# Kernel tuning notes

Hardware: AMD Instinct MI355X
Metric: run time of the kernel (lower is better)

The kernel has to match this reference:

```python
import jax, jax.numpy as jnp
import numpy as np

N_NODES = 40000
N_EDGES = 640000
D = 128
NEG_SLOPE = 0.2
EPS = 0.0  # init_eps=0, learn_eps=False -> constant buffer


def setup_inputs() -> dict:
    key = jax.random.key(0)
    ks = jax.random.split(key, 9)
    return {
        "feat": jax.random.normal(ks[0], (N_NODES, D), dtype=jnp.float32),
        "W_src": jax.random.normal(ks[1], (D, D), dtype=jnp.float32) * 0.1,
        "W_dst": jax.random.normal(ks[2], (D, D), dtype=jnp.float32) * 0.1,
        "W_src2": jax.random.normal(ks[3], (D, D), dtype=jnp.float32) * 0.1,
        "W_dst2": jax.random.normal(ks[4], (D, D), dtype=jnp.float32) * 0.1,
        "attn_l": jax.random.normal(ks[5], (D,), dtype=jnp.float32) * 0.1,
        "attn_r": jax.random.normal(ks[6], (D,), dtype=jnp.float32) * 0.1,
        "src": jax.random.randint(ks[7], (N_EDGES,), 0, N_NODES, dtype=jnp.int32),
        "dst": jax.random.randint(ks[8], (N_EDGES,), 0, N_NODES, dtype=jnp.int32),
    }


def reference(feat, W_src, W_dst, W_src2, W_dst2, attn_l, attn_r, src, dst):
    n = feat.shape[0]
    # Four linear projections (no bias), nn.Linear applies x @ W.T
    fs1 = feat @ W_src.T    # [N, D] -> messages for GIN sum
    fd1 = feat @ W_dst.T    # [N, D] -> self term
    fs2 = feat @ W_src2.T   # [N, D] -> attention-weighted messages
    fd2 = feat @ W_dst2.T   # [N, D]

    # GAT-style per-node attention logits
    el = jnp.sum(fs2 * attn_l, axis=-1)  # [N]
    er = jnp.sum(fd2 * attn_r, axis=-1)  # [N]

    # Per-edge score: u_add_v + leaky_relu
    e = el[src] + er[dst]                                   # [E]
    e = jnp.where(e >= 0, e, NEG_SLOPE * e)

    # edge_softmax: segment-wise softmax over edges grouped by dst
    seg_max = jax.ops.segment_max(e, dst, num_segments=n)   # [N]
    seg_max = jnp.where(jnp.isfinite(seg_max), seg_max, 0.0)
    ex = jnp.exp(e - seg_max[dst])                          # [E]
    denom = jax.ops.segment_sum(ex, dst, num_segments=n)    # [N]
    a = ex / denom[dst]                                     # [E]

    # update_all(copy_u, sum): plain neighbor sum of fs1
    neigh = jax.ops.segment_sum(fs1[src], dst, num_segments=n)            # [N, D]
    # update_all(u_mul_e, sum): attention-weighted sum of fs2
    add_ft = jax.ops.segment_sum(fs2[src] * a[:, None], dst, num_segments=n)  # [N, D]

    rst = (1.0 + EPS) * fd1 + neigh + add_ft
    return rst
```

## Files before the change

kernel.cpp:

```cpp
#include <hip/hip_runtime.h>
#include <math.h>

#define N_NODES 40000
#define N_EDGES 640000
#define D 128
#define NEG_SLOPE 0.2f
#define BCAP 64

typedef __bf16 bf16x8 __attribute__((ext_vector_type(8)));
typedef float f32x4 __attribute__((ext_vector_type(4)));

__device__ __forceinline__ unsigned short f2bf(float f) {
    unsigned int u = __float_as_uint(f);
    return (unsigned short)((u + 0x7fffu + ((u >> 16) & 1u)) >> 16);
}

__global__ void k_init_fill(const float* __restrict__ Ws, const float* __restrict__ Ws2,
                            const float* __restrict__ Wd, const float* __restrict__ Wd2,
                            const float* __restrict__ attn_l, const float* __restrict__ attn_r,
                            unsigned short* __restrict__ Wfrag,
                            float* __restrict__ v_l, float* __restrict__ v_r,
                            const int* __restrict__ src, const int* __restrict__ dst,
                            int* __restrict__ cnt, unsigned short* __restrict__ bucket) {
    if (blockIdx.x >= 193) {
        int e = (blockIdx.x - 193) * 256 + threadIdx.x;
        if (e < N_EDGES) {
            int d = dst[e];
            int slot = atomicAdd(&cnt[d], 1);
            if (slot < BCAP) bucket[(size_t)d * BCAP + slot] = (unsigned short)src[e];
        }
        return;
    }
    if (blockIdx.x == 192) {
        int t = threadIdx.x;
        if (t < 128) {
            float s = 0.0f;
            for (int j = 0; j < D; ++j) s += attn_l[j] * Ws2[j * D + t];
            v_l[t] = s;
        } else {
            int k = t - 128;
            float s = 0.0f;
            for (int j = 0; j < D; ++j) s += attn_r[j] * Wd2[j * D + k];
            v_r[k] = s;
        }
        return;
    }
    int idx = blockIdx.x * 256 + threadIdx.x;
    int e    = idx & 7;
    int lane = (idx >> 3) & 63;
    int ks   = (idx >> 9) & 3;
    int ct   = (idx >> 11) & 7;
    int m    = idx >> 14;
    int col  = ct * 16 + (lane & 15);
    int k    = ks * 32 + (lane >> 4) * 8 + e;
    const float* W = (m == 0) ? Ws : (m == 1) ? Ws2 : Wd;
    Wfrag[idx] = f2bf(W[col * D + k]);
}

__global__ __launch_bounds__(256) void k_gemm(
    const float* __restrict__ feat, const unsigned short* __restrict__ Wfrag,
    const float* __restrict__ vl, const float* __restrict__ vr,
    unsigned int* __restrict__ fsc, unsigned short* __restrict__ fd1b,
    float* __restrict__ el, float* __restrict__ er)
{
    const int m    = blockIdx.x / 625;
    const int tile = blockIdx.x % 625;
    const int lane = threadIdx.x & 63;
    const int wave = threadIdx.x >> 6;
    const int row0 = tile * 64 + wave * 16;
    const int arow = row0 + (lane & 15);
    const int kb   = (lane >> 4) * 8;

    bf16x8 a[4];
    float sl = 0.f, sr = 0.f;
    #pragma unroll
    for (int ks = 0; ks < 4; ++ks) {
        const float* fp = feat + (size_t)arow * D + ks * 32 + kb;
        float4 p = *(const float4*)fp;
        float4 q = *(const float4*)(fp + 4);
        bf16x8 av;
        av[0] = (__bf16)p.x; av[1] = (__bf16)p.y; av[2] = (__bf16)p.z; av[3] = (__bf16)p.w;
        av[4] = (__bf16)q.x; av[5] = (__bf16)q.y; av[6] = (__bf16)q.z; av[7] = (__bf16)q.w;
        a[ks] = av;
        if (m == 0) {
            const float* vlp = vl + ks * 32 + kb;
            const float* vrp = vr + ks * 32 + kb;
            float4 l0 = *(const float4*)vlp, l1 = *(const float4*)(vlp + 4);
            float4 r0 = *(const float4*)vrp, r1 = *(const float4*)(vrp + 4);
            sl += p.x*l0.x + p.y*l0.y + p.z*l0.z + p.w*l0.w
                + q.x*l1.x + q.y*l1.y + q.z*l1.z + q.w*l1.w;
            sr += p.x*r0.x + p.y*r0.y + p.z*r0.z + p.w*r0.w
                + q.x*r1.x + q.y*r1.y + q.z*r1.z + q.w*r1.w;
        }
    }
    if (m == 0) {
        sl += __shfl_xor(sl, 16); sl += __shfl_xor(sl, 32);
        sr += __shfl_xor(sr, 16); sr += __shfl_xor(sr, 32);
        if (lane < 16) { el[row0 + lane] = sl; er[row0 + lane] = sr; }
    }

    const bf16x8* wf = (const bf16x8*)Wfrag + (size_t)(m * 8 * 4) * 64;
    f32x4 acc[8];
    #pragma unroll
    for (int ct = 0; ct < 8; ++ct) acc[ct] = (f32x4){0.f, 0.f, 0.f, 0.f};
    #pragma unroll
    for (int ks = 0; ks < 4; ++ks) {
        #pragma unroll
        for (int ct = 0; ct < 8; ++ct) {
            bf16x8 b = wf[(size_t)(ct * 4 + ks) * 64 + lane];
            acc[ct] = __builtin_amdgcn_mfma_f32_16x16x32_bf16(a[ks], b, acc[ct], 0, 0, 0);
        }
    }

    const int rbase = row0 + (lane >> 4) * 4;
    const int cbase = lane & 15;
    if (m == 2) {
        #pragma unroll
        for (int ct = 0; ct < 8; ++ct)
            #pragma unroll
            for (int r = 0; r < 4; ++r)
                fd1b[(size_t)(rbase + r) * D + ct * 16 + cbase] = f2bf(acc[ct][r]);
    } else {
        const int codd = cbase & 1;
        #pragma unroll
        for (int ct = 0; ct < 8; ++ct) {
            #pragma unroll
            for (int r = 0; r < 4; ++r) {
                unsigned int x = (unsigned int)f2bf(acc[ct][r]);
                unsigned int y = __shfl_xor(x, 1);
                if (!codd) {
                    unsigned int wrd = (y << 16) | x;
                    fsc[(size_t)(rbase + r) * 128 + ct * 16 + cbase + m] = wrd;
                }
            }
        }
    }
}

__global__ __launch_bounds__(256) void k_aggregate(
    const int* __restrict__ cnt, const unsigned short* __restrict__ bucket,
    const float* __restrict__ el, const float* __restrict__ er,
    const uint2* __restrict__ fsc, const unsigned short* __restrict__ fd1b,
    float* __restrict__ out)
{
    const int node = blockIdx.x * 4 + (threadIdx.x >> 6);
    const int lane = threadIdx.x & 63;
    if (node >= N_NODES) return;
    int deg = cnt[node];
    deg = (deg > BCAP) ? BCAP : deg;

    unsigned int u0 = *(const unsigned int*)(fd1b + (size_t)node * D + lane * 2);
    float accx = __uint_as_float(u0 << 16);
    float accy = __uint_as_float(u0 & 0xffff0000u);

    if (deg > 0) {
        const int base = node * BCAP;
        const float ern = er[node];
        int s_l = 0;
        float e = -INFINITY;
        if (lane < deg) {
            s_l = bucket[base + lane];
            e = el[s_l] + ern;
            e = (e >= 0.f) ? e : NEG_SLOPE * e;
        }
        float mx = e;
        #pragma unroll
        for (int w = 32; w >= 1; w >>= 1) mx = fmaxf(mx, __shfl_xor(mx, w));
        float p = (lane < deg) ? __expf(e - mx) : 0.f;
        float ssum = p;
        #pragma unroll
        for (int w = 32; w >= 1; w >>= 1) ssum += __shfl_xor(ssum, w);
        float a_l = p / ssum;

        const int dup = (deg + 15) & ~15;
        for (int i = 0; i < dup; i += 16) {
            uint2 q[16];
            float av[16];
            #pragma unroll
            for (int j = 0; j < 16; ++j) {
                int s = __shfl(s_l, i + j);
                av[j] = __shfl(a_l, i + j);
                q[j] = fsc[(size_t)s * 64 + lane];
            }
            #pragma unroll
            for (int j = 0; j < 16; ++j) {
                float wf = (i + j < deg) ? 1.0f : 0.0f;
                accx += wf * __uint_as_float(q[j].x << 16) + av[j] * __uint_as_float(q[j].y << 16);
                accy += wf * __uint_as_float(q[j].x & 0xffff0000u) + av[j] * __uint_as_float(q[j].y & 0xffff0000u);
            }
        }
    }

    *(float2*)(out + (size_t)node * D + lane * 2) = make_float2(accx, accy);
}

extern "C" void kernel_launch(void* const* d_in, const int* in_sizes, int n_in,
                              void* d_out, int out_size, void* d_ws, size_t ws_size,
                              hipStream_t stream) {
    const float* feat   = (const float*)d_in[0];
    const float* W_src  = (const float*)d_in[1];
    const float* W_dst  = (const float*)d_in[2];
    const float* W_src2 = (const float*)d_in[3];
    const float* W_dst2 = (const float*)d_in[4];
    const float* attn_l = (const float*)d_in[5];
    const float* attn_r = (const float*)d_in[6];
    const int*   src    = (const int*)d_in[7];
    const int*   dst    = (const int*)d_in[8];
    float* out = (float*)d_out;

    char* w = (char*)d_ws;
    float* v_l = (float*)w;                       w += 128 * 4;
    float* v_r = (float*)w;                       w += 128 * 4;
    float* el  = (float*)w;                       w += N_NODES * 4;
    float* er  = (float*)w;                       w += N_NODES * 4;
    int* cnt   = (int*)w;                         w += N_NODES * 4;
    unsigned int* fsc = (unsigned int*)w;         w += (size_t)N_NODES * 128 * 4;
    unsigned short* fd1b = (unsigned short*)w;    w += (size_t)N_NODES * D * 2;
    unsigned short* bucket = (unsigned short*)w;  w += (size_t)N_NODES * BCAP * 2;
    unsigned short* Wfrag = (unsigned short*)w;   w += 3 * 8 * 4 * 64 * 8 * 2;

    hipMemsetAsync(cnt, 0, N_NODES * sizeof(int), stream);

    k_init_fill<<<193 + (N_EDGES + 255) / 256, 256, 0, stream>>>(
        W_src, W_src2, W_dst, W_dst2, attn_l, attn_r, Wfrag, v_l, v_r,
        src, dst, cnt, bucket);

    k_gemm<<<1875, 256, 0, stream>>>(feat, Wfrag, v_l, v_r, fsc, fd1b, el, er);

    k_aggregate<<<(N_NODES + 3) / 4, 256, 0, stream>>>(cnt, bucket, el, er,
                                                       (const uint2*)fsc, fd1b, out);
}
```

Before: 117.4 us.

## Aggregate raw bf16 features first, then project aggregates with post-GEMM

Uses linearity to reorder the computation: the neighbor sums and attention-weighted sums are taken over bf16-converted raw features, and the W_src and W_src2 projections are applied afterwards in a post-aggregation MFMA GEMM that accumulates into the output. The pre-GEMM now computes only the fd1 projection (written to out in fp32) plus the el/er logits, and feat is converted to bf16 in the init kernel. The gather reads 256 B per edge instead of 512 B, but the change adds an extra kernel, bf16 round trips of the aggregates, and a read-modify-write of the output.

```diff
diff --git a/kernel.cpp b/kernel.cpp
--- a/kernel.cpp
+++ b/kernel.cpp
@@ -14,6 +14,8 @@
     unsigned int u = __float_as_uint(f);
     return (unsigned short)((u + 0x7fffu + ((u >> 16) & 1u)) >> 16);
 }
+__device__ __forceinline__ float bflo(unsigned int u) { return __uint_as_float(u << 16); }
+__device__ __forceinline__ float bfhi(unsigned int u) { return __uint_as_float(u & 0xffff0000u); }
 
 __global__ void k_init_fill(const float* __restrict__ Ws, const float* __restrict__ Ws2,
                             const float* __restrict__ Wd, const float* __restrict__ Wd2,
@@ -21,7 +23,23 @@
                             unsigned short* __restrict__ Wfrag,
                             float* __restrict__ v_l, float* __restrict__ v_r,
                             const int* __restrict__ src, const int* __restrict__ dst,
-                            int* __restrict__ cnt, unsigned short* __restrict__ bucket) {
+                            int* __restrict__ cnt, unsigned short* __restrict__ bucket,
+                            const float* __restrict__ feat, unsigned int* __restrict__ featb) {
+    if (blockIdx.x >= 2693) {
+        int t = (blockIdx.x - 2693) * 256 + threadIdx.x;
+        if (t < 640000) {
+            const float* fp = feat + (size_t)t * 8;
+            float4 p = *(const float4*)fp;
+            float4 q = *(const float4*)(fp + 4);
+            uint4 u;
+            u.x = (unsigned int)f2bf(p.x) | ((unsigned int)f2bf(p.y) << 16);
+            u.y = (unsigned int)f2bf(p.z) | ((unsigned int)f2bf(p.w) << 16);
+            u.z = (unsigned int)f2bf(q.x) | ((unsigned int)f2bf(q.y) << 16);
+            u.w = (unsigned int)f2bf(q.z) | ((unsigned int)f2bf(q.w) << 16);
+            *(uint4*)(featb + (size_t)t * 4) = u;
+        }
+        return;
+    }
     if (blockIdx.x >= 193) {
         int e = (blockIdx.x - 193) * 256 + threadIdx.x;
         if (e < N_EDGES) {
@@ -57,17 +75,14 @@
     Wfrag[idx] = f2bf(W[col * D + k]);
 }
 
-__global__ __launch_bounds__(256) void k_gemm(
+__global__ __launch_bounds__(256) void k_gemm_pre(
     const float* __restrict__ feat, const unsigned short* __restrict__ Wfrag,
     const float* __restrict__ vl, const float* __restrict__ vr,
-    unsigned int* __restrict__ fsc, unsigned short* __restrict__ fd1b,
-    float* __restrict__ el, float* __restrict__ er)
+    float* __restrict__ out, float* __restrict__ el, float* __restrict__ er)
 {
-    const int m    = blockIdx.x / 625;
-    const int tile = blockIdx.x % 625;
     const int lane = threadIdx.x & 63;
     const int wave = threadIdx.x >> 6;
-    const int row0 = tile * 64 + wave * 16;
+    const int row0 = blockIdx.x * 64 + wave * 16;
     const int arow = row0 + (lane & 15);
     const int kb   = (lane >> 4) * 8;
 
@@ -82,24 +97,20 @@
         av[0] = (__bf16)p.x; av[1] = (__bf16)p.y; av[2] = (__bf16)p.z; av[3] = (__bf16)p.w;
         av[4] = (__bf16)q.x; av[5] = (__bf16)q.y; av[6] = (__bf16)q.z; av[7] = (__bf16)q.w;
         a[ks] = av;
-        if (m == 0) {
-            const float* vlp = vl + ks * 32 + kb;
-            const float* vrp = vr + ks * 32 + kb;
-            float4 l0 = *(const float4*)vlp, l1 = *(const float4*)(vlp + 4);
-            float4 r0 = *(const float4*)vrp, r1 = *(const float4*)(vrp + 4);
-            sl += p.x*l0.x + p.y*l0.y + p.z*l0.z + p.w*l0.w
-                + q.x*l1.x + q.y*l1.y + q.z*l1.z + q.w*l1.w;
-            sr += p.x*r0.x + p.y*r0.y + p.z*r0.z + p.w*r0.w
-                + q.x*r1.x + q.y*r1.y + q.z*r1.z + q.w*r1.w;
-        }
-    }
-    if (m == 0) {
-        sl += __shfl_xor(sl, 16); sl += __shfl_xor(sl, 32);
-        sr += __shfl_xor(sr, 16); sr += __shfl_xor(sr, 32);
-        if (lane < 16) { el[row0 + lane] = sl; er[row0 + lane] = sr; }
-    }
-
-    const bf16x8* wf = (const bf16x8*)Wfrag + (size_t)(m * 8 * 4) * 64;
+        const float* vlp = vl + ks * 32 + kb;
+        const float* vrp = vr + ks * 32 + kb;
+        float4 l0 = *(const float4*)vlp, l1 = *(const float4*)(vlp + 4);
+        float4 r0 = *(const float4*)vrp, r1 = *(const float4*)(vrp + 4);
+        sl += p.x*l0.x + p.y*l0.y + p.z*l0.z + p.w*l0.w
+            + q.x*l1.x + q.y*l1.y + q.z*l1.z + q.w*l1.w;
+        sr += p.x*r0.x + p.y*r0.y + p.z*r0.z + p.w*r0.w
+            + q.x*r1.x + q.y*r1.y + q.z*r1.z + q.w*r1.w;
+    }
+    sl += __shfl_xor(sl, 16); sl += __shfl_xor(sl, 32);
+    sr += __shfl_xor(sr, 16); sr += __shfl_xor(sr, 32);
+    if (lane < 16) { el[row0 + lane] = sl; er[row0 + lane] = sr; }
+
+    const bf16x8* wf = (const bf16x8*)Wfrag + (size_t)(2 * 8 * 4) * 64;
     f32x4 acc[8];
     #pragma unroll
     for (int ct = 0; ct < 8; ++ct) acc[ct] = (f32x4){0.f, 0.f, 0.f, 0.f};
@@ -114,34 +125,18 @@
 
     const int rbase = row0 + (lane >> 4) * 4;
     const int cbase = lane & 15;
-    if (m == 2) {
-        #pragma unroll
-        for (int ct = 0; ct < 8; ++ct)
-            #pragma unroll
-            for (int r = 0; r < 4; ++r)
-                fd1b[(size_t)(rbase + r) * D + ct * 16 + cbase] = f2bf(acc[ct][r]);
-    } else {
-        const int codd = cbase & 1;
-        #pragma unroll
-        for (int ct = 0; ct < 8; ++ct) {
-            #pragma unroll
-            for (int r = 0; r < 4; ++r) {
-                unsigned int x = (unsigned int)f2bf(acc[ct][r]);
-                unsigned int y = __shfl_xor(x, 1);
-                if (!codd) {
-                    unsigned int wrd = (y << 16) | x;
-                    fsc[(size_t)(rbase + r) * 128 + ct * 16 + cbase + m] = wrd;
-                }
-            }
-        }
-    }
+    #pragma unroll
+    for (int ct = 0; ct < 8; ++ct)
+        #pragma unroll
+        for (int r = 0; r < 4; ++r)
+            out[(size_t)(rbase + r) * D + ct * 16 + cbase] = acc[ct][r];
 }
 
 __global__ __launch_bounds__(256) void k_aggregate(
     const int* __restrict__ cnt, const unsigned short* __restrict__ bucket,
     const float* __restrict__ el, const float* __restrict__ er,
-    const uint2* __restrict__ fsc, const unsigned short* __restrict__ fd1b,
-    float* __restrict__ out)
+    const unsigned int* __restrict__ featb,
+    unsigned int* __restrict__ agg1b, unsigned int* __restrict__ agg2b)
 {
     const int node = blockIdx.x * 4 + (threadIdx.x >> 6);
     const int lane = threadIdx.x & 63;
@@ -149,9 +144,11 @@
     int deg = cnt[node];
     deg = (deg > BCAP) ? BCAP : deg;
 
-    unsigned int u0 = *(const unsigned int*)(fd1b + (size_t)node * D + lane * 2);
-    float accx = __uint_as_float(u0 << 16);
-    float accy = __uint_as_float(u0 & 0xffff0000u);
+    const int q = lane & 15;
+    const int g = lane >> 4;
+    float A1[8], A2[8];
+    #pragma unroll
+    for (int c = 0; c < 8; ++c) { A1[c] = 0.f; A2[c] = 0.f; }
 
     if (deg > 0) {
         const int base = node * BCAP;
@@ -174,24 +171,94 @@
 
         const int dup = (deg + 15) & ~15;
         for (int i = 0; i < dup; i += 16) {
-            uint2 q[16];
-            float av[16];
+            uint4 v[4];
+            float av[4], wf[4];
             #pragma unroll
-            for (int j = 0; j < 16; ++j) {
-                int s = __shfl(s_l, i + j);
-                av[j] = __shfl(a_l, i + j);
-                q[j] = fsc[(size_t)s * 64 + lane];
+            for (int j = 0; j < 4; ++j) {
+                int eidx = i + j * 4 + g;
+                int s = __shfl(s_l, eidx);
+                av[j] = __shfl(a_l, eidx);
+                wf[j] = (eidx < deg) ? 1.0f : 0.0f;
+                v[j] = *(const uint4*)(featb + (size_t)s * 64 + q * 4);
             }
             #pragma unroll
-            for (int j = 0; j < 16; ++j) {
-                float wf = (i + j < deg) ? 1.0f : 0.0f;
-                accx += wf * __uint_as_float(q[j].x << 16) + av[j] * __uint_as_float(q[j].y << 16);
-                accy += wf * __uint_as_float(q[j].x & 0xffff0000u) + av[j] * __uint_as_float(q[j].y & 0xffff0000u);
+            for (int j = 0; j < 4; ++j) {
+                float x0 = bflo(v[j].x), x1 = bfhi(v[j].x);
+                float x2 = bflo(v[j].y), x3 = bfhi(v[j].y);
+                float x4 = bflo(v[j].z), x5 = bfhi(v[j].z);
+                float x6 = bflo(v[j].w), x7 = bfhi(v[j].w);
+                A1[0] += wf[j] * x0; A2[0] += av[j] * x0;
+                A1[1] += wf[j] * x1; A2[1] += av[j] * x1;
+                A1[2] += wf[j] * x2; A2[2] += av[j] * x2;
+                A1[3] += wf[j] * x3; A2[3] += av[j] * x3;
+                A1[4] += wf[j] * x4; A2[4] += av[j] * x4;
+                A1[5] += wf[j] * x5; A2[5] += av[j] * x5;
+                A1[6] += wf[j] * x6; A2[6] += av[j] * x6;
+                A1[7] += wf[j] * x7; A2[7] += av[j] * x7;
             }
         }
-    }
-
-    *(float2*)(out + (size_t)node * D + lane * 2) = make_float2(accx, accy);
+        #pragma unroll
+        for (int c = 0; c < 8; ++c) {
+            A1[c] += __shfl_xor(A1[c], 16); A1[c] += __shfl_xor(A1[c], 32);
+            A2[c] += __shfl_xor(A2[c], 16); A2[c] += __shfl_xor(A2[c], 32);
+        }
+    }
+
+    if (lane < 16) {
+        uint4 u1, u2;
+        u1.x = (unsigned int)f2bf(A1[0]) | ((unsigned int)f2bf(A1[1]) << 16);
+        u1.y = (unsigned int)f2bf(A1[2]) | ((unsigned int)f2bf(A1[3]) << 16);
+        u1.z = (unsigned int)f2bf(A1[4]) | ((unsigned int)f2bf(A1[5]) << 16);
+        u1.w = (unsigned int)f2bf(A1[6]) | ((unsigned int)f2bf(A1[7]) << 16);
+        u2.x = (unsigned int)f2bf(A2[0]) | ((unsigned int)f2bf(A2[1]) << 16);
+        u2.y = (unsigned int)f2bf(A2[2]) | ((unsigned int)f2bf(A2[3]) << 16);
+        u2.z = (unsigned int)f2bf(A2[4]) | ((unsigned int)f2bf(A2[5]) << 16);
+        u2.w = (unsigned int)f2bf(A2[6]) | ((unsigned int)f2bf(A2[7]) << 16);
+        *(uint4*)(agg1b + (size_t)node * 64 + q * 4) = u1;
+        *(uint4*)(agg2b + (size_t)node * 64 + q * 4) = u2;
+    }
+}
+
+__global__ __launch_bounds__(256) void k_gemm_post(
+    const unsigned int* __restrict__ agg1b, const unsigned int* __restrict__ agg2b,
+    const unsigned short* __restrict__ Wfrag, float* __restrict__ out)
+{
+    const int lane = threadIdx.x & 63;
+    const int wave = threadIdx.x >> 6;
+    const int row0 = blockIdx.x * 64 + wave * 16;
+    const int arow = row0 + (lane & 15);
+    const int kb   = (lane >> 4) * 8;
+
+    bf16x8 a1[4], a2[4];
+    #pragma unroll
+    for (int ks = 0; ks < 4; ++ks) {
+        a1[ks] = *(const bf16x8*)((const unsigned short*)agg1b + (size_t)arow * D + ks * 32 + kb);
+        a2[ks] = *(const bf16x8*)((const unsigned short*)agg2b + (size_t)arow * D + ks * 32 + kb);
+    }
+
+    const bf16x8* wf0 = (const bf16x8*)Wfrag;
+    const bf16x8* wf1 = (const bf16x8*)Wfrag + (size_t)(8 * 4) * 64;
+    f32x4 acc[8];
+    #pragma unroll
+    for (int ct = 0; ct < 8; ++ct) acc[ct] = (f32x4){0.f, 0.f, 0.f, 0.f};
+    #pragma unroll
+    for (int ks = 0; ks < 4; ++ks) {
+        #pragma unroll
+        for (int ct = 0; ct < 8; ++ct) {
+            acc[ct] = __builtin_amdgcn_mfma_f32_16x16x32_bf16(a1[ks], wf0[(size_t)(ct * 4 + ks) * 64 + lane], acc[ct], 0, 0, 0);
+            acc[ct] = __builtin_amdgcn_mfma_f32_16x16x32_bf16(a2[ks], wf1[(size_t)(ct * 4 + ks) * 64 + lane], acc[ct], 0, 0, 0);
+        }
+    }
+
+    const int rbase = row0 + (lane >> 4) * 4;
+    const int cbase = lane & 15;
+    #pragma unroll
+    for (int ct = 0; ct < 8; ++ct)
+        #pragma unroll
+        for (int r = 0; r < 4; ++r) {
+            size_t o = (size_t)(rbase + r) * D + ct * 16 + cbase;
+            out[o] += acc[ct][r];
+        }
 }
 
 extern "C" void kernel_launch(void* const* d_in, const int* in_sizes, int n_in,
@@ -214,19 +281,22 @@
     float* el  = (float*)w;                       w += N_NODES * 4;
     float* er  = (float*)w;                       w += N_NODES * 4;
     int* cnt   = (int*)w;                         w += N_NODES * 4;
-    unsigned int* fsc = (unsigned int*)w;         w += (size_t)N_NODES * 128 * 4;
-    unsigned short* fd1b = (unsigned short*)w;    w += (size_t)N_NODES * D * 2;
+    unsigned int* featb = (unsigned int*)w;       w += (size_t)N_NODES * 64 * 4;
+    unsigned int* agg1b = (unsigned int*)w;       w += (size_t)N_NODES * 64 * 4;
+    unsigned int* agg2b = (unsigned int*)w;       w += (size_t)N_NODES * 64 * 4;
     unsigned short* bucket = (unsigned short*)w;  w += (size_t)N_NODES * BCAP * 2;
     unsigned short* Wfrag = (unsigned short*)w;   w += 3 * 8 * 4 * 64 * 8 * 2;
 
     hipMemsetAsync(cnt, 0, N_NODES * sizeof(int), stream);
 
-    k_init_fill<<<193 + (N_EDGES + 255) / 256, 256, 0, stream>>>(
+    k_init_fill<<<5193, 256, 0, stream>>>(
         W_src, W_src2, W_dst, W_dst2, attn_l, attn_r, Wfrag, v_l, v_r,
-        src, dst, cnt, bucket);
-
-    k_gemm<<<1875, 256, 0, stream>>>(feat, Wfrag, v_l, v_r, fsc, fd1b, el, er);
+        src, dst, cnt, bucket, feat, featb);
+
+    k_gemm_pre<<<625, 256, 0, stream>>>(feat, Wfrag, v_l, v_r, out, el, er);
 
     k_aggregate<<<(N_NODES + 3) / 4, 256, 0, stream>>>(cnt, bucket, el, er,
-                                                       (const uint2*)fsc, fd1b, out);
-}
+                                                       featb, agg1b, agg2b);
+
+    k_gemm_post<<<625, 256, 0, stream>>>(agg1b, agg2b, Wfrag, out);
+}
```

New measurement: 101.8 us. 1.15x faster.
